# Kernel optimization log

Measured on AMD Instinct MI355X. Metric: run time of the kernel, lower is better.

The kernel has to match this reference:

```python
import jax, jax.numpy as jnp
import numpy as np

B_J0 = 0.01   # baseline threshold
DT = 1.0
BETA = 1.8    # adaptation strength
LENS = 0.5
SCALE = 6.0
HIGHT = 0.15
GAMMA = 0.5


def _gauss(x, mu, sigma):
    return jnp.exp(-(x - mu) ** 2 / (2.0 * sigma ** 2)) / jnp.sqrt(2.0 * jnp.pi) / sigma


@jax.custom_vjp
def spike_fn(x):
    return (x > 0).astype(x.dtype)


def _spike_fwd(x):
    return spike_fn(x), x


def _spike_bwd(x, g):
    # multi-gaussian surrogate gradient (config.gradient_type == 'MG')
    temp = (_gauss(x, 0.0, LENS) * (1.0 + HIGHT)
            - _gauss(x, LENS, SCALE * LENS) * HIGHT
            - _gauss(x, -LENS, SCALE * LENS) * HIGHT)
    return (g * temp * GAMMA,)


spike_fn.defvjp(_spike_fwd, _spike_bwd)


def setup_inputs() -> dict:
    key = jax.random.key(0)
    ks = jax.random.split(key, 20)
    Bt, T, I, H, O = 256, 250, 700, 128, 20
    f32 = jnp.float32
    return {
        'x': jax.random.uniform(ks[0], (Bt, T, I), dtype=f32),
        'mask': jnp.ones((2, H, H), dtype=f32),
        'w_ih1': (jax.random.normal(ks[1], (I, H), dtype=f32) / np.sqrt(I).astype(np.float32)),
        'b_ih1': jnp.zeros((H,), f32),
        'w_h1h1': (jax.random.normal(ks[2], (H, H), dtype=f32) / np.sqrt(H).astype(np.float32)),
        'b_h1h1': jnp.zeros((H,), f32),
        'w_h1h2': (jax.random.normal(ks[3], (H, H), dtype=f32) / np.sqrt(H).astype(np.float32)),
        'b_h1h2': jnp.zeros((H,), f32),
        'w_h2h2': (jax.random.normal(ks[4], (H, H), dtype=f32) / np.sqrt(H).astype(np.float32)),
        'b_h2h2': jnp.zeros((H,), f32),
        'w_h2o': (jax.random.normal(ks[5], (H, O), dtype=f32) / np.sqrt(H).astype(np.float32)),
        'b_h2o': jnp.zeros((O,), f32),
        'tau_adp_h1': 150.0 + 10.0 * jax.random.normal(ks[6], (H,), dtype=f32),
        'tau_adp_h2': 150.0 + 10.0 * jax.random.normal(ks[7], (H,), dtype=f32),
        'tau_m_h1': 20.0 + 5.0 * jax.random.normal(ks[8], (H,), dtype=f32),
        'tau_m_h2': 20.0 + 5.0 * jax.random.normal(ks[9], (H,), dtype=f32),
        'tau_m_o': 20.0 + 5.0 * jax.random.normal(ks[10], (O,), dtype=f32),
        'hid1_mem0': jax.random.uniform(ks[11], (Bt, H), dtype=f32),
        'hid2_mem0': jax.random.uniform(ks[12], (Bt, H), dtype=f32),
        'out_mem0': jax.random.uniform(ks[13], (Bt, O), dtype=f32),
    }


def _forward(x, mask, w_ih1, b_ih1, w_h1h1, b_h1h1, w_h1h2, b_h1h2,
             w_h2h2, b_h2h2, w_h2o, b_h2o, tau_adp_h1, tau_adp_h2,
             tau_m_h1, tau_m_h2, tau_m_o, hid1_mem0, hid2_mem0, out_mem0):
    Bt, T, _ = x.shape
    H = w_ih1.shape[1]
    O = w_h2o.shape[1]
    # dropout mask applied to recurrent weights (weights stored [in, out])
    w11 = w_h1h1 * mask[0]
    w22 = w_h2h2 * mask[1]
    a1 = jnp.exp(-DT / tau_m_h1)
    r1 = jnp.exp(-DT / tau_adp_h1)
    a2 = jnp.exp(-DT / tau_m_h2)
    r2 = jnp.exp(-DT / tau_adp_h2)
    ao = jnp.exp(-DT / tau_m_o)
    # precompute input projection for all timesteps: [T, B, H]
    xin = jnp.einsum('bti,ih->tbh', x, w_ih1) + b_ih1

    def step(carry, inps):
        h1m, h1s, h2m, h2s, om, b1, b2, acc, s1, s2 = carry
        xt, t = inps
        # layer 1 (adaptive LIF)
        i1 = xt + h1s @ w11 + b_h1h1
        b1 = r1 * b1 + (1.0 - r1) * h1s
        B1 = B_J0 + BETA * b1
        h1m = h1m * a1 + (1.0 - a1) * i1 - B1 * h1s * DT
        h1s = spike_fn(h1m - B1)
        s1 = s1 + h1s
        # layer 2 (adaptive LIF)
        i2 = h1s @ w_h1h2 + b_h1h2 + h2s @ w22 + b_h2h2
        b2 = r2 * b2 + (1.0 - r2) * h2s
        B2 = B_J0 + BETA * b2
        h2m = h2m * a2 + (1.0 - a2) * i2 - B2 * h2s * DT
        h2s = spike_fn(h2m - B2)
        s2 = s2 + h2s
        # leaky-integrator readout (no spike)
        io = h2s @ w_h2o + b_h2o
        om = om * ao + (1.0 - ao) * io
        acc = acc + jnp.where(t > 10, jax.nn.softmax(om, axis=-1), 0.0)
        return (h1m, h1s, h2m, h2s, om, b1, b2, acc, s1, s2), None

    zH = jnp.zeros((Bt, H), x.dtype)
    carry0 = (hid1_mem0, zH, hid2_mem0, zH, out_mem0,
              jnp.full((Bt, H), B_J0, x.dtype), jnp.full((Bt, H), B_J0, x.dtype),
              jnp.zeros((Bt, O), x.dtype), zH, zH)
    carry, _ = jax.lax.scan(step, carry0, (xin, jnp.arange(T)))
    output, s1, s2 = carry[7], carry[8], carry[9]
    A_norm = jnp.sum(jnp.abs(w11)) + jnp.sum(jnp.abs(w22))
    return output, s1 / T, s2 / T, A_norm


def reference(x, mask, w_ih1, b_ih1, w_h1h1, b_h1h1, w_h1h2, b_h1h2,
              w_h2h2, b_h2h2, w_h2o, b_h2o, tau_adp_h1, tau_adp_h2,
              tau_m_h1, tau_m_h2, tau_m_o, hid1_mem0, hid2_mem0, out_mem0):
    return _forward(x, mask, w_ih1, b_ih1, w_h1h1, b_h1h1, w_h1h2, b_h1h2,
                    w_h2h2, b_h2h2, w_h2o, b_h2o, tau_adp_h1, tau_adp_h2,
                    tau_m_h1, tau_m_h2, tau_m_o, hid1_mem0, hid2_mem0, out_mem0)
```

## Files before the change

### kernel.cpp

```cpp
#include <hip/hip_runtime.h>
#include <math.h>

#define TT 250
#define BT 256
#define HN 128
#define ON 20
#define KIN 700
#define NKT 22

#define XIN_OFF 0
#define WPKH_OFF 8192000
#define WPKL_OFF 8237056

typedef __attribute__((ext_vector_type(8))) short bf16x8;
typedef __attribute__((ext_vector_type(4))) float f32x4;

__device__ __forceinline__ unsigned short bf16rne(float f) {
    unsigned u = __float_as_uint(f);
    unsigned r = u + 0x7fffu + ((u >> 16) & 1u);
    return (unsigned short)(r >> 16);
}
__device__ __forceinline__ void hilo(float v, short& h, short& l) {
    unsigned short hh = bf16rne(v);
    float vh = __uint_as_float((unsigned)hh << 16);
    h = (short)hh;
    l = (short)bf16rne(v - vh);
}

#define LBAR() do { asm volatile("s_waitcnt lgkmcnt(0)" ::: "memory"); \
                    __builtin_amdgcn_s_barrier();                      \
                    asm volatile("" ::: "memory"); } while (0)

__device__ __forceinline__ void gl_lds16(const void* g, void* l) {
    __builtin_amdgcn_global_load_lds(
        (const __attribute__((address_space(1))) unsigned int*)g,
        (__attribute__((address_space(3))) unsigned int*)l, 16, 0, 0);
}

__global__ __launch_bounds__(256) void packw(const float* __restrict__ w,
                                             unsigned short* __restrict__ ph,
                                             unsigned short* __restrict__ pl) {
    int i = blockIdx.x * 256 + threadIdx.x;
    int k = i >> 7, c = i & 127;
    float v = (k < KIN) ? w[k * HN + c] : 0.f;
    short h, l;
    hilo(v, h, l);
    int dst = (((k >> 5) * 8 + (c >> 4)) * 64 + (((k >> 3) & 3) * 16 + (c & 15))) * 8 + (k & 7);
    ph[dst] = (unsigned short)h;
    pl[dst] = (unsigned short)l;
}

__device__ __forceinline__ void stage_kt(const unsigned short* __restrict__ wph,
                                         const unsigned short* __restrict__ wpl,
                                         void* buf, int kt, int tid) {
    const char* sh = (const char*)wph + kt * 8192 + tid * 16;
    const char* sl = (const char*)wpl + kt * 8192 + tid * 16;
    char* b = (char*)buf;
    const int wb = (tid >> 6) * 1024;
    gl_lds16(sh,        b + wb);
    gl_lds16(sh + 4096, b + wb + 4096);
    gl_lds16(sl,        b + wb + 8192);
    gl_lds16(sl + 4096, b + wb + 12288);
}

__device__ __forceinline__ void loadx8(float* av, const float* p, bool tailq3) {
    *(float4*)&av[0] = *(const float4*)p;
    if (tailq3) {
        av[4] = 0.f; av[5] = 0.f; av[6] = 0.f; av[7] = 0.f;
    } else {
        *(float4*)&av[4] = *(const float4*)(p + 4);
    }
}

__global__ __launch_bounds__(256, 4) void gemm_in(const float* __restrict__ x,
        const unsigned short* __restrict__ wph, const unsigned short* __restrict__ wpl,
        const float* __restrict__ bias1, const float* __restrict__ bias2,
        float* __restrict__ xin) {
    __shared__ __align__(16) unsigned char wbuf[2][16384];
    const int tid = threadIdx.x;
    const int w = tid >> 6, lane = tid & 63;
    const int q = lane >> 4, li = lane & 15;
    const long mrow = (long)blockIdx.x * 64 + w * 16 + li;
    const float* xr = x + mrow * KIN + q * 8;

    f32x4 acc[8];
#pragma unroll
    for (int nt = 0; nt < 8; nt++) acc[nt] = (f32x4){0.f, 0.f, 0.f, 0.f};

    stage_kt(wph, wpl, wbuf[0], 0, tid);
    float av[8];
    loadx8(av, xr, false);
    __syncthreads();

#pragma unroll 2
    for (int kt = 0; kt < NKT; kt++) {
        if (kt + 1 < NKT)
            stage_kt(wph, wpl, wbuf[(kt + 1) & 1], kt + 1, tid);
        float avn[8];
        if (kt + 1 < NKT)
            loadx8(avn, xr + (kt + 1) * 32, (kt + 1 == NKT - 1) && (q == 3));

        bf16x8 ah, al;
#pragma unroll
        for (int j = 0; j < 8; j++) {
            short h, l;
            hilo(av[j], h, l);
            ah[j] = h; al[j] = l;
        }

        const bf16x8* cv = (const bf16x8*)&wbuf[kt & 1][0];
#pragma unroll 2
        for (int nt = 0; nt < 8; nt++) {
            bf16x8 bh = cv[nt * 64 + lane];
            bf16x8 bl = cv[512 + nt * 64 + lane];
            acc[nt] = __builtin_amdgcn_mfma_f32_16x16x32_bf16(ah, bh, acc[nt], 0, 0, 0);
            acc[nt] = __builtin_amdgcn_mfma_f32_16x16x32_bf16(al, bh, acc[nt], 0, 0, 0);
            acc[nt] = __builtin_amdgcn_mfma_f32_16x16x32_bf16(ah, bl, acc[nt], 0, 0, 0);
        }

        if (kt + 1 < NKT) {
#pragma unroll
            for (int j = 0; j < 8; j++) av[j] = avn[j];
        }
        __syncthreads();
    }

    float b12[8];
#pragma unroll
    for (int nt = 0; nt < 8; nt++) {
        int c = nt * 16 + li;
        b12[nt] = bias1[c] + bias2[c];
    }
#pragma unroll
    for (int r = 0; r < 4; r++) {
        int m = blockIdx.x * 64 + w * 16 + q * 4 + r;
        int bq = (int)(((unsigned long long)m * 67109ull) >> 24);
        int tt = m - bq * 250;
        float* dst = xin + ((size_t)tt * BT + bq) * HN;
#pragma unroll
        for (int nt = 0; nt < 8; nt++) dst[nt * 16 + li] = acc[nt][r] + b12[nt];
    }
}

__global__ __launch_bounds__(512, 1) void snn_scan(
    const float* __restrict__ xin, const float* __restrict__ mask,
    const float* __restrict__ w_h1h1, const float* __restrict__ w_h1h2,
    const float* __restrict__ b_h1h2, const float* __restrict__ w_h2h2,
    const float* __restrict__ b_h2h2, const float* __restrict__ w_h2o,
    const float* __restrict__ b_h2o, const float* __restrict__ tau_adp1,
    const float* __restrict__ tau_adp2, const float* __restrict__ taum1,
    const float* __restrict__ taum2, const float* __restrict__ taumo,
    const float* __restrict__ h1m0, const float* __restrict__ h2m0,
    const float* __restrict__ om0, float* __restrict__ out) {

    __shared__ __align__(16) unsigned short sA1[2 * 2048];
    __shared__ __align__(16) unsigned short sA2[2048];
    __shared__ float omb[16 * ON];
    __shared__ float red[8];

    const int tid = threadIdx.x;
    const int w = tid >> 6, lane = tid & 63;
    const int q = lane >> 4, li = lane & 15;
    const int col = w * 16 + li;
    const int r0 = blockIdx.x * 16;

    bf16x8 h11[4], l11[4], h22[4], l22[4], h12[4], l12[4], hO[4], lO[4];
    const int ocol = (w == 6) ? li : 16 + li;
    const bool oval = (w >= 6) && (ocol < ON);
    float pn = 0.f;
#pragma unroll
    for (int kt = 0; kt < 4; kt++) {
#pragma unroll
        for (int j = 0; j < 8; j++) {
            const int k = kt * 32 + q * 8 + j;
            const int idx = k * HN + col;
            float v11 = w_h1h1[idx] * mask[idx];
            float v22 = w_h2h2[idx] * mask[HN * HN + idx];
            float v12 = w_h1h2[idx];
            pn += fabsf(v11) + fabsf(v22);
            short hh, ll;
            hilo(v11, hh, ll); h11[kt][j] = hh; l11[kt][j] = ll;
            hilo(v22, hh, ll); h22[kt][j] = hh; l22[kt][j] = ll;
            hilo(v12, hh, ll); h12[kt][j] = hh; l12[kt][j] = ll;
            float vO = oval ? w_h2o[k * ON + ocol] : 0.f;
            hilo(vO, hh, ll); hO[kt][j] = hh; lO[kt][j] = ll;
        }
    }

    const float a1 = expf(-1.f / taum1[col]);
    const float r1 = expf(-1.f / tau_adp1[col]);
    const float a2 = expf(-1.f / taum2[col]);
    const float r2 = expf(-1.f / tau_adp2[col]);
    const float cc2 = b_h1h2[col] + b_h2h2[col];
    float h1m[4], h2m[4], b1[4], b2[4], c1[4], c2n[4];
    unsigned s1bits = 0, s2bits = 0;
#pragma unroll
    for (int r = 0; r < 4; r++) {
        h1m[r] = h1m0[(r0 + q * 4 + r) * HN + col];
        h2m[r] = h2m0[(r0 + q * 4 + r) * HN + col];
        b1[r] = 0.01f; b2[r] = 0.01f; c1[r] = 0.f; c2n[r] = 0.f;
    }
    const float ao = oval ? expf(-1.f / taumo[ocol]) : 0.f;
    const float bo = oval ? b_h2o[ocol] : 0.f;
    float om[4];
#pragma unroll
    for (int r = 0; r < 4; r++)
        om[r] = oval ? om0[(r0 + q * 4 + r) * ON + ocol] : 0.f;
    const int sm = lane >> 2, ob = (lane & 3) * 5;
    float accs[5] = {0.f, 0.f, 0.f, 0.f, 0.f};

    {
        unsigned* z1 = (unsigned*)sA1;
        unsigned* z2 = (unsigned*)sA2;
        z1[tid] = 0u; z1[tid + 512] = 0u;
        z2[tid] = 0u; z2[tid + 512] = 0u;
    }

#pragma unroll
    for (int off = 32; off > 0; off >>= 1) pn += __shfl_down(pn, off);
    if (lane == 0) red[w] = pn;
    __syncthreads();
    if (tid == 0 && blockIdx.x == 0) {
        float s = 0.f;
#pragma unroll
        for (int i = 0; i < 8; i++) s += red[i];
        out[70656] = s;
    }

    const int wbase = (w >> 1) * 512 + (((2 * w + (li >> 3)) & 3) * 16 + q * 4) * 8 + (li & 7);

    const bf16x8* sa1v = (const bf16x8*)sA1;
    const bf16x8* sa2v = (const bf16x8*)sA2;
    const unsigned short ONE = 0x3F80u;

    bf16x8 f1c[4];
    const bf16x8 zf = {0, 0, 0, 0, 0, 0, 0, 0};
#pragma unroll
    for (int kt = 0; kt < 4; kt++) f1c[kt] = zf;

    float xt[4], xtn[4];
#pragma unroll
    for (int r = 0; r < 4; r++)
        xt[r] = xin[((size_t)0 * BT + r0 + q * 4 + r) * HN + col];

    for (int t = 0; t < TT; t++) {
        const int wb = ((t + 1) & 1) * 2048;

        const int tn = (t + 1 < TT) ? t + 1 : t;
#pragma unroll
        for (int r = 0; r < 4; r++)
            xtn[r] = xin[((size_t)tn * BT + r0 + q * 4 + r) * HN + col];

        bf16x8 f2[4];
#pragma unroll
        for (int kt = 0; kt < 4; kt++) f2[kt] = sa2v[kt * 64 + lane];
        f32x4 aI = {0.f, 0.f, 0.f, 0.f}, aG = {0.f, 0.f, 0.f, 0.f};
#pragma unroll
        for (int kt = 0; kt < 4; kt++) {
            aI = __builtin_amdgcn_mfma_f32_16x16x32_bf16(f1c[kt], h11[kt], aI, 0, 0, 0);
            aI = __builtin_amdgcn_mfma_f32_16x16x32_bf16(f1c[kt], l11[kt], aI, 0, 0, 0);
            aG = __builtin_amdgcn_mfma_f32_16x16x32_bf16(f2[kt], h22[kt], aG, 0, 0, 0);
            aG = __builtin_amdgcn_mfma_f32_16x16x32_bf16(f2[kt], l22[kt], aG, 0, 0, 0);
        }
        if (w >= 6) {
            f32x4 aO = {0.f, 0.f, 0.f, 0.f};
#pragma unroll
            for (int kt = 0; kt < 4; kt++) {
                aO = __builtin_amdgcn_mfma_f32_16x16x32_bf16(f2[kt], hO[kt], aO, 0, 0, 0);
                aO = __builtin_amdgcn_mfma_f32_16x16x32_bf16(f2[kt], lO[kt], aO, 0, 0, 0);
            }
            if (t >= 1) {
#pragma unroll
                for (int r = 0; r < 4; r++) {
                    om[r] = ao * om[r] + (1.f - ao) * (bo + aO[r]);
                    if (oval) omb[(q * 4 + r) * ON + ocol] = om[r];
                }
            }
        }
#pragma unroll
        for (int r = 0; r < 4; r++) {
            const float sv = (float)((s1bits >> r) & 1u);
            const float i1 = xt[r] + aI[r];
            b1[r] = r1 * b1[r] + (1.f - r1) * sv;
            const float B = 0.01f + 1.8f * b1[r];
            h1m[r] = a1 * h1m[r] + (1.f - a1) * i1 - B * sv;
            const bool sp = (h1m[r] - B) > 0.f;
            s1bits = sp ? (s1bits | (1u << r)) : (s1bits & ~(1u << r));
            c1[r] += sp ? 1.f : 0.f;
            sA1[wb + wbase + r * 8] = sp ? ONE : (unsigned short)0;
        }
        LBAR();

        bf16x8 g1[4];
#pragma unroll
        for (int kt = 0; kt < 4; kt++) g1[kt] = sa1v[(wb >> 3) + kt * 64 + lane];
        f32x4 aJ = {0.f, 0.f, 0.f, 0.f};
#pragma unroll
        for (int kt = 0; kt < 4; kt++) {
            aJ = __builtin_amdgcn_mfma_f32_16x16x32_bf16(g1[kt], h12[kt], aJ, 0, 0, 0);
            aJ = __builtin_amdgcn_mfma_f32_16x16x32_bf16(g1[kt], l12[kt], aJ, 0, 0, 0);
        }
        if (w == 7 && t >= 12) {
            float v[5], e[5];
            float mx = -1e30f;
#pragma unroll
            for (int i = 0; i < 5; i++) { v[i] = omb[sm * ON + ob + i]; mx = fmaxf(mx, v[i]); }
            mx = fmaxf(mx, __shfl_xor(mx, 1));
            mx = fmaxf(mx, __shfl_xor(mx, 2));
            float se = 0.f;
#pragma unroll
            for (int i = 0; i < 5; i++) { e[i] = __expf(v[i] - mx); se += e[i]; }
            se += __shfl_xor(se, 1);
            se += __shfl_xor(se, 2);
            const float inv = 1.f / se;
#pragma unroll
            for (int i = 0; i < 5; i++) accs[i] += e[i] * inv;
        }
#pragma unroll
        for (int r = 0; r < 4; r++) {
            const float sv = (float)((s2bits >> r) & 1u);
            const float i2 = aJ[r] + aG[r] + cc2;
            b2[r] = r2 * b2[r] + (1.f - r2) * sv;
            const float B = 0.01f + 1.8f * b2[r];
            h2m[r] = a2 * h2m[r] + (1.f - a2) * i2 - B * sv;
            const bool sp = (h2m[r] - B) > 0.f;
            s2bits = sp ? (s2bits | (1u << r)) : (s2bits & ~(1u << r));
            c2n[r] += sp ? 1.f : 0.f;
            sA2[wbase + r * 8] = sp ? ONE : (unsigned short)0;
        }
#pragma unroll
        for (int kt = 0; kt < 4; kt++) f1c[kt] = g1[kt];
#pragma unroll
        for (int r = 0; r < 4; r++) xt[r] = xtn[r];
        LBAR();
    }

    if (w >= 6) {
        bf16x8 f2[4];
#pragma unroll
        for (int kt = 0; kt < 4; kt++) f2[kt] = sa2v[kt * 64 + lane];
        f32x4 aO = {0.f, 0.f, 0.f, 0.f};
#pragma unroll
        for (int kt = 0; kt < 4; kt++) {
            aO = __builtin_amdgcn_mfma_f32_16x16x32_bf16(f2[kt], hO[kt], aO, 0, 0, 0);
            aO = __builtin_amdgcn_mfma_f32_16x16x32_bf16(f2[kt], lO[kt], aO, 0, 0, 0);
        }
#pragma unroll
        for (int r = 0; r < 4; r++) {
            om[r] = ao * om[r] + (1.f - ao) * (bo + aO[r]);
            if (oval) omb[(q * 4 + r) * ON + ocol] = om[r];
        }
    }
    __syncthreads();
    if (w == 7) {
        float v[5], e[5];
        float mx = -1e30f;
#pragma unroll
        for (int i = 0; i < 5; i++) { v[i] = omb[sm * ON + ob + i]; mx = fmaxf(mx, v[i]); }
        mx = fmaxf(mx, __shfl_xor(mx, 1));
        mx = fmaxf(mx, __shfl_xor(mx, 2));
        float se = 0.f;
#pragma unroll
        for (int i = 0; i < 5; i++) { e[i] = __expf(v[i] - mx); se += e[i]; }
        se += __shfl_xor(se, 1);
        se += __shfl_xor(se, 2);
        const float inv = 1.f / se;
#pragma unroll
        for (int i = 0; i < 5; i++) out[(r0 + sm) * ON + ob + i] = accs[i] + e[i] * inv;
    }
#pragma unroll
    for (int r = 0; r < 4; r++) {
        out[5120 + (r0 + q * 4 + r) * HN + col] = c1[r] * (1.f / 250.f);
        out[37888 + (r0 + q * 4 + r) * HN + col] = c2n[r] * (1.f / 250.f);
    }
}

extern "C" void kernel_launch(void* const* d_in, const int* in_sizes, int n_in,
                              void* d_out, int out_size, void* d_ws, size_t ws_size,
                              hipStream_t stream) {
    const float* x        = (const float*)d_in[0];
    const float* mask     = (const float*)d_in[1];
    const float* w_ih1    = (const float*)d_in[2];
    const float* b_ih1    = (const float*)d_in[3];
    const float* w_h1h1   = (const float*)d_in[4];
    const float* b_h1h1   = (const float*)d_in[5];
    const float* w_h1h2   = (const float*)d_in[6];
    const float* b_h1h2   = (const float*)d_in[7];
    const float* w_h2h2   = (const float*)d_in[8];
    const float* b_h2h2   = (const float*)d_in[9];
    const float* w_h2o    = (const float*)d_in[10];
    const float* b_h2o    = (const float*)d_in[11];
    const float* tau_adp1 = (const float*)d_in[12];
    const float* tau_adp2 = (const float*)d_in[13];
    const float* taum1    = (const float*)d_in[14];
    const float* taum2    = (const float*)d_in[15];
    const float* taumo    = (const float*)d_in[16];
    const float* h1m0     = (const float*)d_in[17];
    const float* h2m0     = (const float*)d_in[18];
    const float* om0      = (const float*)d_in[19];
    float* out = (float*)d_out;
    float* ws  = (float*)d_ws;

    float* xin = ws + XIN_OFF;
    unsigned short* wph = (unsigned short*)(ws + WPKH_OFF);
    unsigned short* wpl = (unsigned short*)(ws + WPKL_OFF);

    packw<<<352, 256, 0, stream>>>(w_ih1, wph, wpl);
    gemm_in<<<1000, 256, 0, stream>>>(x, wph, wpl, b_ih1, b_h1h1, xin);
    snn_scan<<<16, 512, 0, stream>>>(xin, mask, w_h1h1, w_h1h2, b_h1h2, w_h2h2,
                                     b_h2h2, w_h2o, b_h2o, tau_adp1, tau_adp2,
                                     taum1, taum2, taumo, h1m0, h2m0, om0, out);
}
```

Baseline: 636.4 us.

## Double rows per GEMM block and simplify scan buffering and barriers

The input GEMM now computes 128 rows per block (two 64-row chunks sharing each staged weight tile), halving the grid and the weight re-staging traffic per row, with launch bounds relaxed for more registers. The scan kernel drops its double-buffered layer-1 spike LDS and the x prefetch into the next step, uses plain __syncthreads instead of the lgkmcnt barrier macro, and moves the softmax accumulation from wave 7 to wave 0. The GEMM change targets LDS/global weight reuse; the scan changes trade latency hiding (prefetch) for lower register and LDS use, and the softmax move may shift load off the output waves. The sA2 read for the recurrent step now follows a barrier, so correctness relies on the single-buffered ordering being preserved.

Measured after the change: 609.7 us. -4.2%, faster.

```diff
diff --git a/kernel.cpp b/kernel.cpp
--- a/kernel.cpp
+++ b/kernel.cpp
@@ -26,10 +26,6 @@
     h = (short)hh;
     l = (short)bf16rne(v - vh);
 }
-
-#define LBAR() do { asm volatile("s_waitcnt lgkmcnt(0)" ::: "memory"); \
-                    __builtin_amdgcn_s_barrier();                      \
-                    asm volatile("" ::: "memory"); } while (0)
 
 __device__ __forceinline__ void gl_lds16(const void* g, void* l) {
     __builtin_amdgcn_global_load_lds(
@@ -72,7 +68,7 @@
     }
 }
 
-__global__ __launch_bounds__(256, 4) void gemm_in(const float* __restrict__ x,
+__global__ __launch_bounds__(256, 2) void gemm_in(const float* __restrict__ x,
         const unsigned short* __restrict__ wph, const unsigned short* __restrict__ wpl,
         const float* __restrict__ bias1, const float* __restrict__ bias2,
         float* __restrict__ xin) {
@@ -80,47 +76,45 @@
     const int tid = threadIdx.x;
     const int w = tid >> 6, lane = tid & 63;
     const int q = lane >> 4, li = lane & 15;
-    const long mrow = (long)blockIdx.x * 64 + w * 16 + li;
-    const float* xr = x + mrow * KIN + q * 8;
-
-    f32x4 acc[8];
-#pragma unroll
-    for (int nt = 0; nt < 8; nt++) acc[nt] = (f32x4){0.f, 0.f, 0.f, 0.f};
+    const long mbase = (long)blockIdx.x * 128;
+    const float* xr0 = x + (mbase + w * 16 + li) * KIN + q * 8;
+
+    f32x4 acc[2][8];
+#pragma unroll
+    for (int c = 0; c < 2; c++)
+#pragma unroll
+        for (int nt = 0; nt < 8; nt++) acc[c][nt] = (f32x4){0.f, 0.f, 0.f, 0.f};
 
     stage_kt(wph, wpl, wbuf[0], 0, tid);
-    float av[8];
-    loadx8(av, xr, false);
+    float av[2][8];
+    loadx8(av[0], xr0, false);
+    loadx8(av[1], xr0 + 64 * KIN, false);
     __syncthreads();
 
-#pragma unroll 2
     for (int kt = 0; kt < NKT; kt++) {
         if (kt + 1 < NKT)
             stage_kt(wph, wpl, wbuf[(kt + 1) & 1], kt + 1, tid);
-        float avn[8];
-        if (kt + 1 < NKT)
-            loadx8(avn, xr + (kt + 1) * 32, (kt + 1 == NKT - 1) && (q == 3));
-
-        bf16x8 ah, al;
-#pragma unroll
-        for (int j = 0; j < 8; j++) {
-            short h, l;
-            hilo(av[j], h, l);
-            ah[j] = h; al[j] = l;
-        }
-
         const bf16x8* cv = (const bf16x8*)&wbuf[kt & 1][0];
-#pragma unroll 2
-        for (int nt = 0; nt < 8; nt++) {
-            bf16x8 bh = cv[nt * 64 + lane];
-            bf16x8 bl = cv[512 + nt * 64 + lane];
-            acc[nt] = __builtin_amdgcn_mfma_f32_16x16x32_bf16(ah, bh, acc[nt], 0, 0, 0);
-            acc[nt] = __builtin_amdgcn_mfma_f32_16x16x32_bf16(al, bh, acc[nt], 0, 0, 0);
-            acc[nt] = __builtin_amdgcn_mfma_f32_16x16x32_bf16(ah, bl, acc[nt], 0, 0, 0);
-        }
-
-        if (kt + 1 < NKT) {
-#pragma unroll
-            for (int j = 0; j < 8; j++) av[j] = avn[j];
+#pragma unroll
+        for (int c = 0; c < 2; c++) {
+            bf16x8 ah, al;
+#pragma unroll
+            for (int j = 0; j < 8; j++) {
+                short h, l;
+                hilo(av[c][j], h, l);
+                ah[j] = h; al[j] = l;
+            }
+            if (kt + 1 < NKT)
+                loadx8(av[c], xr0 + c * (64 * KIN) + (kt + 1) * 32,
+                       (kt + 1 == NKT - 1) && (q == 3));
+#pragma unroll
+            for (int nt = 0; nt < 8; nt++) {
+                bf16x8 bh = cv[nt * 64 + lane];
+                bf16x8 bl = cv[512 + nt * 64 + lane];
+                acc[c][nt] = __builtin_amdgcn_mfma_f32_16x16x32_bf16(ah, bh, acc[c][nt], 0, 0, 0);
+                acc[c][nt] = __builtin_amdgcn_mfma_f32_16x16x32_bf16(al, bh, acc[c][nt], 0, 0, 0);
+                acc[c][nt] = __builtin_amdgcn_mfma_f32_16x16x32_bf16(ah, bl, acc[c][nt], 0, 0, 0);
+            }
         }
         __syncthreads();
     }
@@ -132,17 +126,20 @@
         b12[nt] = bias1[c] + bias2[c];
     }
 #pragma unroll
-    for (int r = 0; r < 4; r++) {
-        int m = blockIdx.x * 64 + w * 16 + q * 4 + r;
-        int bq = (int)(((unsigned long long)m * 67109ull) >> 24);
-        int tt = m - bq * 250;
-        float* dst = xin + ((size_t)tt * BT + bq) * HN;
-#pragma unroll
-        for (int nt = 0; nt < 8; nt++) dst[nt * 16 + li] = acc[nt][r] + b12[nt];
-    }
-}
-
-__global__ __launch_bounds__(512, 1) void snn_scan(
+    for (int c = 0; c < 2; c++) {
+#pragma unroll
+        for (int r = 0; r < 4; r++) {
+            long m = mbase + c * 64 + w * 16 + q * 4 + r;
+            int bq = (int)(((unsigned long long)m * 67109ull) >> 24);
+            int tt = (int)m - bq * 250;
+            float* dst = xin + ((size_t)tt * BT + bq) * HN;
+#pragma unroll
+            for (int nt = 0; nt < 8; nt++) dst[nt * 16 + li] = acc[c][nt][r] + b12[nt];
+        }
+    }
+}
+
+__global__ __launch_bounds__(512, 2) void snn_scan(
     const float* __restrict__ xin, const float* __restrict__ mask,
     const float* __restrict__ w_h1h1, const float* __restrict__ w_h1h2,
     const float* __restrict__ b_h1h2, const float* __restrict__ w_h2h2,
@@ -153,7 +150,7 @@
     const float* __restrict__ h1m0, const float* __restrict__ h2m0,
     const float* __restrict__ om0, float* __restrict__ out) {
 
-    __shared__ __align__(16) unsigned short sA1[2 * 2048];
+    __shared__ __align__(16) unsigned short sA1[2048];
     __shared__ __align__(16) unsigned short sA2[2048];
     __shared__ float omb[16 * ON];
     __shared__ float red[8];
@@ -212,8 +209,8 @@
     {
         unsigned* z1 = (unsigned*)sA1;
         unsigned* z2 = (unsigned*)sA2;
-        z1[tid] = 0u; z1[tid + 512] = 0u;
-        z2[tid] = 0u; z2[tid + 512] = 0u;
+        z1[tid & 511] = 0u; z1[(tid & 511) + 512] = 0u;
+        z2[tid & 511] = 0u; z2[(tid & 511) + 512] = 0u;
     }
 
 #pragma unroll
@@ -233,23 +230,18 @@
     const bf16x8* sa2v = (const bf16x8*)sA2;
     const unsigned short ONE = 0x3F80u;
 
-    bf16x8 f1c[4];
+    bf16x8 g1[4];
     const bf16x8 zf = {0, 0, 0, 0, 0, 0, 0, 0};
 #pragma unroll
-    for (int kt = 0; kt < 4; kt++) f1c[kt] = zf;
-
-    float xt[4], xtn[4];
-#pragma unroll
-    for (int r = 0; r < 4; r++)
-        xt[r] = xin[((size_t)0 * BT + r0 + q * 4 + r) * HN + col];
+    for (int kt = 0; kt < 4; kt++) g1[kt] = zf;
+
+    const float* xp = xin + (size_t)(r0 + q * 4) * HN + col;
 
     for (int t = 0; t < TT; t++) {
-        const int wb = ((t + 1) & 1) * 2048;
-
-        const int tn = (t + 1 < TT) ? t + 1 : t;
-#pragma unroll
-        for (int r = 0; r < 4; r++)
-            xtn[r] = xin[((size_t)tn * BT + r0 + q * 4 + r) * HN + col];
+        float xt[4];
+#pragma unroll
+        for (int r = 0; r < 4; r++) xt[r] = xp[r * HN];
+        xp += BT * HN;
 
         bf16x8 f2[4];
 #pragma unroll
@@ -257,8 +249,8 @@
         f32x4 aI = {0.f, 0.f, 0.f, 0.f}, aG = {0.f, 0.f, 0.f, 0.f};
 #pragma unroll
         for (int kt = 0; kt < 4; kt++) {
-            aI = __builtin_amdgcn_mfma_f32_16x16x32_bf16(f1c[kt], h11[kt], aI, 0, 0, 0);
-            aI = __builtin_amdgcn_mfma_f32_16x16x32_bf16(f1c[kt], l11[kt], aI, 0, 0, 0);
+            aI = __builtin_amdgcn_mfma_f32_16x16x32_bf16(g1[kt], h11[kt], aI, 0, 0, 0);
+            aI = __builtin_amdgcn_mfma_f32_16x16x32_bf16(g1[kt], l11[kt], aI, 0, 0, 0);
             aG = __builtin_amdgcn_mfma_f32_16x16x32_bf16(f2[kt], h22[kt], aG, 0, 0, 0);
             aG = __builtin_amdgcn_mfma_f32_16x16x32_bf16(f2[kt], l22[kt], aG, 0, 0, 0);
         }
@@ -287,20 +279,19 @@
             const bool sp = (h1m[r] - B) > 0.f;
             s1bits = sp ? (s1bits | (1u << r)) : (s1bits & ~(1u << r));
             c1[r] += sp ? 1.f : 0.f;
-            sA1[wb + wbase + r * 8] = sp ? ONE : (unsigned short)0;
-        }
-        LBAR();
-
-        bf16x8 g1[4];
-#pragma unroll
-        for (int kt = 0; kt < 4; kt++) g1[kt] = sa1v[(wb >> 3) + kt * 64 + lane];
+            sA1[wbase + r * 8] = sp ? ONE : (unsigned short)0;
+        }
+        __syncthreads();
+
+#pragma unroll
+        for (int kt = 0; kt < 4; kt++) g1[kt] = sa1v[kt * 64 + lane];
         f32x4 aJ = {0.f, 0.f, 0.f, 0.f};
 #pragma unroll
         for (int kt = 0; kt < 4; kt++) {
             aJ = __builtin_amdgcn_mfma_f32_16x16x32_bf16(g1[kt], h12[kt], aJ, 0, 0, 0);
             aJ = __builtin_amdgcn_mfma_f32_16x16x32_bf16(g1[kt], l12[kt], aJ, 0, 0, 0);
         }
-        if (w == 7 && t >= 12) {
+        if (w == 0 && t >= 12) {
             float v[5], e[5];
             float mx = -1e30f;
 #pragma unroll
@@ -328,11 +319,7 @@
             c2n[r] += sp ? 1.f : 0.f;
             sA2[wbase + r * 8] = sp ? ONE : (unsigned short)0;
         }
-#pragma unroll
-        for (int kt = 0; kt < 4; kt++) f1c[kt] = g1[kt];
-#pragma unroll
-        for (int r = 0; r < 4; r++) xt[r] = xtn[r];
-        LBAR();
+        __syncthreads();
     }
 
     if (w >= 6) {
@@ -352,7 +339,7 @@
         }
     }
     __syncthreads();
-    if (w == 7) {
+    if (w == 0) {
         float v[5], e[5];
         float mx = -1e30f;
 #pragma unroll
@@ -406,7 +393,7 @@
     unsigned short* wpl = (unsigned short*)(ws + WPKL_OFF);
 
     packw<<<352, 256, 0, stream>>>(w_ih1, wph, wpl);
-    gemm_in<<<1000, 256, 0, stream>>>(x, wph, wpl, b_ih1, b_h1h1, xin);
+    gemm_in<<<500, 256, 0, stream>>>(x, wph, wpl, b_ih1, b_h1h1, xin);
     snn_scan<<<16, 512, 0, stream>>>(xin, mask, w_h1h1, w_h1h2, b_h1h2, w_h2h2,
                                      b_h2h2, w_h2o, b_h2o, tau_adp1, tau_adp2,
                                      taum1, taum2, taumo, h1m0, h2m0, om0, out);
```
